# Kernel tuning notes

Measured on AMD Instinct MI355X. Metric: run time of the kernel, lower is better.

## Reference

```python
import jax, jax.numpy as jnp
import numpy as np

NUM_HEADS = 8
EPS = 1e-12  # torch F.normalize eps


def setup_inputs() -> dict:
    key = jax.random.key(0)
    k1, k2, k3 = jax.random.split(key, 3)
    B, N, C = 8, 4096, 768
    x = jax.random.normal(k1, (B, N, C), dtype=jnp.float32)
    Wqkv = jax.random.normal(k2, (C, 3 * C), dtype=jnp.float32) * 0.02
    temperature = jnp.ones((NUM_HEADS, 1, 1), dtype=jnp.float32)
    Wproj = jax.random.normal(k3, (C, C), dtype=jnp.float32) * 0.02
    bproj = jnp.zeros((C,), dtype=jnp.float32)
    return {"x": x, "Wqkv": Wqkv, "temperature": temperature,
            "Wproj": Wproj, "bproj": bproj}


def _l2norm(t):
    # torch F.normalize(dim=-1): x / max(||x||, eps)
    n = jnp.sqrt(jnp.sum(t * t, axis=-1, keepdims=True))
    return t / jnp.maximum(n, EPS)


def reference(x, Wqkv, temperature, Wproj, bproj):
    B, N, C = x.shape
    H = NUM_HEADS
    Ch = C // H
    qkv = (x @ Wqkv).reshape(B, N, 3, H, Ch)
    qkv = qkv.transpose(2, 0, 3, 1, 4)           # (3, B, H, N, Ch)
    q, k, v = qkv[0], qkv[1], qkv[2]
    # transpose(-2,-1): attend over channels -> (B, H, Ch, N)
    q = jnp.swapaxes(q, -2, -1)
    k = jnp.swapaxes(k, -2, -1)
    v = jnp.swapaxes(v, -2, -1)
    q = _l2norm(q)
    k = _l2norm(k)
    # (B, H, Ch, Ch) channel-attention scores, scaled by learned temperature
    attn = jnp.einsum('bhcn,bhdn->bhcd', q, k) * temperature
    attn = jax.nn.softmax(attn, axis=-1)
    out = jnp.einsum('bhcd,bhdn->bhcn', attn, v)  # (B, H, Ch, N)
    out = out.transpose(0, 3, 1, 2).reshape(B, N, C)
    return out @ Wproj + bproj
```

## Files before the change

### kernel.cpp

```cpp
#include <hip/hip_runtime.h>
#include <cstdint>
#include <cstddef>

typedef unsigned short u16;
typedef short bf16x8 __attribute__((ext_vector_type(8)));
typedef unsigned short u16x4 __attribute__((ext_vector_type(4)));
typedef unsigned short u16x8 __attribute__((ext_vector_type(8)));
typedef float f32x4 __attribute__((ext_vector_type(4)));

#define EPSN 1e-12f

__device__ __forceinline__ u16 f2bf(float f) {
  uint32_t u = __builtin_bit_cast(uint32_t, f);
  u += 0x7FFFu + ((u >> 16) & 1u);
  return (u16)(u >> 16);
}
__device__ __forceinline__ float bf2f(u16 h) {
  uint32_t u = ((uint32_t)h) << 16;
  return __builtin_bit_cast(float, u);
}

__device__ __forceinline__ void gll16(const u16* g, u16* l) {
  __builtin_amdgcn_global_load_lds(
      (const __attribute__((address_space(1))) void*)g,
      (__attribute__((address_space(3))) void*)l, 16, 0, 0);
}

__global__ __launch_bounds__(256)
void k_cvtT(const float* __restrict__ x, u16* __restrict__ Xh,
            u16* __restrict__ XhT) {
  __shared__ u16 tr[64][68];
  const int tid = threadIdx.x;
  const int t0 = blockIdx.x * 64, k0 = blockIdx.y * 64, b = blockIdx.z;
  const size_t base = ((size_t)b * 4096 + t0) * 768 + k0;
#pragma unroll
  for (int p = 0; p < 4; p++) {
    const int r = (tid >> 4) + p * 16;
    const int c = (tid & 15) * 4;
    f32x4 v = *(const f32x4*)(x + base + (size_t)r * 768 + c);
    u16x4 o;
#pragma unroll
    for (int e = 0; e < 4; e++) o[e] = f2bf(v[e]);
    *(u16x4*)(Xh + base + (size_t)r * 768 + c) = o;
    tr[c + 0][r] = o[0];
    tr[c + 1][r] = o[1];
    tr[c + 2][r] = o[2];
    tr[c + 3][r] = o[3];
  }
  __syncthreads();
  const size_t tbase = ((size_t)b * 768 + k0) * 4096 + t0;
#pragma unroll
  for (int p = 0; p < 4; p++) {
    const int kk = (tid >> 4) + p * 16;
    const int ts = (tid & 15) * 4;
    u16x4 o;
#pragma unroll
    for (int e = 0; e < 4; e++) o[e] = tr[kk][ts + e];
    *(u16x4*)(XhT + tbase + (size_t)kk * 4096 + ts) = o;
  }
}

__global__ __launch_bounds__(256)
void k_wt(const float* __restrict__ W, u16* __restrict__ Wt, u16* __restrict__ Wvh) {
  __shared__ float tile[32][33];
  const int j0 = blockIdx.x * 32;
  const int k0 = blockIdx.y * 32;
  const int tx = threadIdx.x & 31;
  const int ty = threadIdx.x >> 5;
#pragma unroll
  for (int r = 0; r < 4; r++) {
    float v = W[(size_t)(k0 + ty + r * 8) * 2304 + j0 + tx];
    tile[ty + r * 8][tx] = v;
    if (j0 >= 1536)
      Wvh[(size_t)(k0 + ty + r * 8) * 768 + (j0 - 1536) + tx] = f2bf(v);
  }
  __syncthreads();
  if (j0 < 1536) {
#pragma unroll
    for (int r = 0; r < 4; r++)
      Wt[(size_t)(j0 + ty + r * 8) * 768 + k0 + tx] = f2bf(tile[tx][ty + r * 8]);
  }
}

template <int OUTF32B, int TRI>
__global__ __launch_bounds__(256, 3)
void k_gemm(const u16* __restrict__ A, const u16* __restrict__ Btp,
            void* __restrict__ Cp, const float* __restrict__ bias,
            int K, int lda, int ldb, int ldc,
            long aZ, long bZ, long cZ, int zK, long kss) {
  const int gx = gridDim.x, gy = gridDim.y;
  int f = blockIdx.x + gx * (blockIdx.y + gy * blockIdx.z);
  const int total = gx * gy * gridDim.z;
  const int q = total >> 3, rr = total & 7;
  const int xcd = f & 7, kk0 = f >> 3;
  f = (xcd < rr ? xcd * (q + 1) : rr * (q + 1) + (xcd - rr) * q) + kk0;
  const int bx = f % gx;
  const int tmp = f / gx;
  const int by = tmp % gy;
  const int bz = tmp / gy;

  int m0, n0;
  if constexpr (TRI) {
    const int ty = (bx >= 20) ? 5 : (bx >= 18) ? 4 : (bx >= 15) ? 3
                 : (bx >= 11) ? 2 : (bx >= 6) ? 1 : 0;
    const int txi = ty + (bx - (ty * 6 - (ty * (ty - 1)) / 2));
    m0 = ty * 128;
    n0 = txi * 128;
  } else {
    m0 = by * 128;
    n0 = bx * 128;
  }
  const int z = bz;
  const int bb = z / zK, ss = z % zK;
  const u16* Az = A + (long)bb * aZ + (long)ss * kss;
  const u16* Btz = Btp + (long)bb * bZ + (long)ss * kss;

  __shared__ u16 As[128 * 32];
  __shared__ u16 Bs[128 * 32];
  const int tid = threadIdx.x;
  const int lane = tid & 63;
  const int wid = tid >> 6;
  const int wr = wid >> 1, wc = wid & 1;
  const int fm = lane & 15, kg = lane >> 4;

  const int lr = lane >> 2;
  const int gk = (lane & 3) ^ ((lane >> 3) & 3);
  const u16* gA0 = Az + (size_t)(m0 + wid * 32 + lr) * lda + gk * 8;
  const u16* gA1 = gA0 + (size_t)16 * lda;
  const u16* gB0 = Btz + (size_t)(n0 + wid * 32 + lr) * ldb + gk * 8;
  const u16* gB1 = gB0 + (size_t)16 * ldb;
  u16* lA0 = As + wid * 1024;
  u16* lA1 = lA0 + 512;
  u16* lB0 = Bs + wid * 1024;
  u16* lB1 = lB0 + 512;
  const int kq = (kg ^ ((fm >> 1) & 3)) * 8;

  f32x4 acc[4][4] = {};
  for (int k0 = 0; k0 < K; k0 += 32) {
    __syncthreads();
    gll16(gA0, lA0);
    gll16(gA1, lA1);
    gll16(gB0, lB0);
    gll16(gB1, lB1);
    gA0 += 32; gA1 += 32; gB0 += 32; gB1 += 32;
    __syncthreads();
    bf16x8 af[4], bfr[4];
#pragma unroll
    for (int i = 0; i < 4; i++)
      af[i] = *(const bf16x8*)&As[(wr * 64 + i * 16 + fm) * 32 + kq];
#pragma unroll
    for (int j = 0; j < 4; j++)
      bfr[j] = *(const bf16x8*)&Bs[(wc * 64 + j * 16 + fm) * 32 + kq];
#pragma unroll
    for (int i = 0; i < 4; i++)
#pragma unroll
      for (int j = 0; j < 4; j++)
        acc[i][j] = __builtin_amdgcn_mfma_f32_16x16x32_bf16(af[i], bfr[j], acc[i][j], 0, 0, 0);
  }

  if constexpr (OUTF32B) {
    float* C = (float*)Cp + (long)z * cZ;
#pragma unroll
    for (int j = 0; j < 4; j++) {
      const int col = n0 + wc * 64 + j * 16 + fm;
      const float bj = bias[col];
#pragma unroll
      for (int i = 0; i < 4; i++) {
        const int r0 = m0 + wr * 64 + i * 16 + kg * 4;
#pragma unroll
        for (int r = 0; r < 4; r++)
          C[(size_t)(r0 + r) * ldc + col] = acc[i][j][r] + bj;
      }
    }
  } else {
    const int rb = TRI ? 0 : m0;
    const int cb = TRI ? 0 : n0;
    const int ld = TRI ? 128 : ldc;
    u16* C = (u16*)Cp + (long)z * cZ + (TRI ? (long)bx * 16384 : 0L);
#pragma unroll
    for (int j = 0; j < 4; j++) {
      const int col = cb + wc * 64 + j * 16 + fm;
#pragma unroll
      for (int i = 0; i < 4; i++) {
        const int r0 = rb + wr * 64 + i * 16 + kg * 4;
#pragma unroll
        for (int r = 0; r < 4; r++)
          C[(size_t)(r0 + r) * ld + col] = f2bf(acc[i][j][r]);
      }
    }
  }
}

__global__ __launch_bounds__(256)
void k_red(const u16* __restrict__ P, u16* __restrict__ O) {
  const int b = blockIdx.y;
  const int ti = blockIdx.x / 6, tj = blockIdx.x % 6;
  const bool mirror = ti > tj;
  const int a = mirror ? tj : ti;
  const int c2 = mirror ? ti : tj;
  const int src = a * 6 - (a * (a - 1)) / 2 + (c2 - a);
  __shared__ u16 lt[128 * 128];
  const int tid = threadIdx.x;
  const int r = tid >> 1;
  const int ch = (tid & 1) * 64;
  float acc[64] = {};
  for (int s = 0; s < 4; s++) {
    const u16* p = P + ((size_t)(b * 4 + s) * 344064 + (size_t)src * 16384);
    __syncthreads();
#pragma unroll
    for (int it = 0; it < 8; it++) {
      const int idx = (tid + it * 256) * 8;
      *(u16x8*)&lt[idx] = *(const u16x8*)(p + idx);
    }
    __syncthreads();
    if (!mirror) {
#pragma unroll
      for (int e = 0; e < 64; e++) acc[e] += bf2f(lt[r * 128 + ch + e]);
    } else {
#pragma unroll
      for (int e = 0; e < 64; e++) acc[e] += bf2f(lt[(ch + e) * 128 + r]);
    }
  }
  u16* o = O + (size_t)b * 589824 + (size_t)(ti * 128 + r) * 768 + tj * 128 + ch;
#pragma unroll
  for (int v8 = 0; v8 < 8; v8++) {
    u16x8 w;
#pragma unroll
    for (int e = 0; e < 8; e++) w[e] = f2bf(acc[v8 * 8 + e]);
    *(u16x8*)(o + v8 * 8) = w;
  }
}

__global__ __launch_bounds__(256)
void k_score(const u16* __restrict__ Tm, const u16* __restrict__ Wt,
             const float* __restrict__ temperature, float* __restrict__ Aattn) {
  const int h = blockIdx.x, b = blockIdx.y;
  const int bh = b * 8 + h;
  __shared__ u16 As[96 * 32];
  __shared__ u16 Bs[96 * 32];
  __shared__ u16 Dt2[96 * 32];
  __shared__ u16 Dwq[96 * 32];
  __shared__ float Gs[96 * 96];
  __shared__ float nqs[96], nks[96], invk[96];

  const int tid = threadIdx.x;
  const int lane = tid & 63;
  const int wid = tid >> 6;
  const int wr = wid >> 1, wc = wid & 1;
  const int fm = lane & 15, kg = lane >> 4;
  const int lr = lane >> 2;
  const int gkS = (lane & 3) ^ ((lane >> 3) & 3);
  const int gkL = (lane & 3);
  const int kq = (kg ^ ((fm >> 1) & 3)) * 8;

  const u16* baseT1 = Tm + (size_t)b * 1179648 + (size_t)(h * 96) * 768;
  const u16* baseT2 = baseT1 + (size_t)768 * 768;
  const u16* baseWq = Wt + (size_t)(h * 96) * 768;
  const u16* baseWk = baseWq + (size_t)768 * 768;

  const u16* gsrc;
  u16* ldst;
  int gblk = gkS;
  if (wid == 0) { gsrc = baseT1; ldst = As; }
  else if (wid == 1) { gsrc = baseWk; ldst = Bs; }
  else if (wid == 2) { gsrc = baseT2; ldst = Dt2; gblk = gkL; }
  else { gsrc = baseWq; ldst = Dwq; gblk = gkL; }

  f32x4 acc[3][3] = {};
  float nqa = 0.f, nka = 0.f;
  const int sw1 = (tid < 96) ? ((tid >> 1) & 3) : 0;
  const int sw2 = (tid >= 128 && tid < 224) ? (((tid - 128) >> 1) & 3) : 0;

  for (int k0 = 0; k0 < 768; k0 += 32) {
    __syncthreads();
#pragma unroll
    for (int c = 0; c < 6; c++) {
      gll16(gsrc + (size_t)(c * 16 + lr) * 768 + k0 + gblk * 8,
            ldst + c * 512);
    }
    __syncthreads();
    bf16x8 af[3], bfr[3];
#pragma unroll
    for (int i = 0; i < 3; i++)
      af[i] = *(const bf16x8*)&As[(wr * 48 + i * 16 + fm) * 32 + kq];
#pragma unroll
    for (int j = 0; j < 3; j++)
      bfr[j] = *(const bf16x8*)&Bs[(wc * 48 + j * 16 + fm) * 32 + kq];
#pragma unroll
    for (int i = 0; i < 3; i++)
#pragma unroll
      for (int j = 0; j < 3; j++)
        acc[i][j] = __builtin_amdgcn_mfma_f32_16x16x32_bf16(af[i], bfr[j], acc[i][j], 0, 0, 0);
    if (tid < 96) {
#pragma unroll
      for (int g = 0; g < 4; g++) {
        u16x8 av = *(const u16x8*)&As[tid * 32 + (g ^ sw1) * 8];
        u16x8 w = *(const u16x8*)&Dwq[tid * 32 + g * 8];
#pragma unroll
        for (int e = 0; e < 8; e++) nqa += bf2f(av[e]) * bf2f(w[e]);
      }
    } else if (tid >= 128 && tid < 224) {
      const int d = tid - 128;
#pragma unroll
      for (int g = 0; g < 4; g++) {
        u16x8 av = *(const u16x8*)&Bs[d * 32 + (g ^ sw2) * 8];
        u16x8 w = *(const u16x8*)&Dt2[d * 32 + g * 8];
#pragma unroll
        for (int e = 0; e < 8; e++) nka += bf2f(av[e]) * bf2f(w[e]);
      }
    }
  }

  if (tid < 96) nqs[tid] = nqa;
  if (tid >= 128 && tid < 224) nks[tid - 128] = nka;
#pragma unroll
  for (int i = 0; i < 3; i++)
#pragma unroll
    for (int j = 0; j < 3; j++)
#pragma unroll
      for (int r = 0; r < 4; r++)
        Gs[(wr * 48 + i * 16 + kg * 4 + r) * 96 + wc * 48 + j * 16 + fm] = acc[i][j][r];
  __syncthreads();
  if (tid < 96) invk[tid] = 1.0f / fmaxf(sqrtf(nks[tid]), EPSN);
  __syncthreads();
  if (tid < 96) {
    const int c = tid;
    const float iq = temperature[h] / fmaxf(sqrtf(nqs[c]), EPSN);
    float sv[96];
    float m = -1e30f;
#pragma unroll
    for (int d = 0; d < 96; d++) {
      float s = Gs[c * 96 + d] * iq * invk[d];
      sv[d] = s;
      m = fmaxf(m, s);
    }
    float sum = 0.f;
#pragma unroll
    for (int d = 0; d < 96; d++) {
      float e = __expf(sv[d] - m);
      sv[d] = e;
      sum += e;
    }
    const float inv = 1.0f / sum;
    float* dst = Aattn + (size_t)bh * 9216 + (size_t)c * 96;
#pragma unroll
    for (int d = 0; d < 96; d++) dst[d] = sv[d] * inv;
  }
}

__global__ __launch_bounds__(256)
void k_weff(const float* __restrict__ Aattn, const float* __restrict__ Wproj,
            u16* __restrict__ Weff) {
  const int jt = blockIdx.x, h = blockIdx.y, b = blockIdx.z;
  const int bh = b * 8 + h;
  __shared__ float As2[9216];
  const int tid = threadIdx.x;
  for (int idx = tid; idx < 9216; idx += 256)
    As2[idx] = Aattn[(size_t)bh * 9216 + idx];
  __syncthreads();
  const int jloc = tid & 127;
  const int half = tid >> 7;
  const int j = jt * 128 + jloc;
  float acc[48] = {};
  for (int c = 0; c < 96; c++) {
    const float w = Wproj[(size_t)(h * 96 + c) * 768 + j];
    const f32x4* ar = (const f32x4*)&As2[c * 96 + half * 48];
#pragma unroll
    for (int v4 = 0; v4 < 12; v4++) {
      f32x4 av = ar[v4];
      acc[v4 * 4 + 0] += w * av[0];
      acc[v4 * 4 + 1] += w * av[1];
      acc[v4 * 4 + 2] += w * av[2];
      acc[v4 * 4 + 3] += w * av[3];
    }
  }
  u16* dst = Weff + ((size_t)b * 768 + j) * 768 + h * 96 + half * 48;
#pragma unroll
  for (int v4 = 0; v4 < 12; v4++) {
    u16x4 o;
    o[0] = f2bf(acc[v4 * 4 + 0]);
    o[1] = f2bf(acc[v4 * 4 + 1]);
    o[2] = f2bf(acc[v4 * 4 + 2]);
    o[3] = f2bf(acc[v4 * 4 + 3]);
    *(u16x4*)(dst + v4 * 4) = o;
  }
}

extern "C" void kernel_launch(void* const* d_in, const int* in_sizes, int n_in,
                              void* d_out, int out_size, void* d_ws, size_t ws_size,
                              hipStream_t stream) {
  const float* x = (const float*)d_in[0];
  const float* Wqkv = (const float*)d_in[1];
  const float* temp = (const float*)d_in[2];
  const float* Wproj = (const float*)d_in[3];
  const float* bproj = (const float*)d_in[4];
  float* out = (float*)d_out;

  char* ws = (char*)d_ws;
  u16* Xh = (u16*)ws;
  u16* XhT = (u16*)(ws + 50331648);
  u16* Wt = (u16*)(ws + 100663296);
  u16* Wvh = (u16*)(ws + 103022592);
  u16* XtXp = (u16*)(ws + 104202240);
  u16* XtXbf = (u16*)(ws + 141950976);
  u16* T = (u16*)(ws + 151388160);
  u16* WeffT = (u16*)(ws + 151388160);
  u16* WcompT = (u16*)(ws + 160825344);
  float* Aattn = (float*)(ws + 170262528);

  k_cvtT<<<dim3(64, 12, 8), 256, 0, stream>>>(x, Xh, XhT);
  k_wt<<<dim3(72, 24), 256, 0, stream>>>(Wqkv, Wt, Wvh);
  k_gemm<0, 1><<<dim3(21, 1, 32), 256, 0, stream>>>(
      XhT, XhT, (void*)XtXp, nullptr, 1024, 4096, 4096, 0,
      3145728L, 3145728L, 344064L, 4, 1024L);
  k_red<<<dim3(36, 8), 256, 0, stream>>>(XtXp, XtXbf);
  k_gemm<0, 0><<<dim3(6, 12, 8), 256, 0, stream>>>(
      Wt, XtXbf, (void*)T, nullptr, 768, 768, 768, 768,
      0L, 589824L, 1179648L, 1, 0L);
  k_score<<<dim3(8, 8), 256, 0, stream>>>(T, Wt, temp, Aattn);
  k_weff<<<dim3(6, 8, 8), 256, 0, stream>>>(Aattn, Wproj, WeffT);
  k_gemm<0, 0><<<dim3(6, 6, 8), 256, 0, stream>>>(
      WeffT, Wvh, (void*)WcompT, nullptr, 768, 768, 768, 768,
      589824L, 0L, 589824L, 1, 0L);
  k_gemm<1, 0><<<dim3(6, 32, 8), 256, 0, stream>>>(
      Xh, WcompT, out, bproj, 768, 768, 768, 768,
      3145728L, 589824L, 3145728L, 1, 0L);
}
```

Baseline: 304.5 us.

## Triple-buffer LDS tiles in bf16 GEMM to overlap global loads with MFMA

Replaces the single-buffered LDS staging in the GEMM kernel with a three-slot ring buffer. Tiles for k-step t+2 are prefetched with global_load_lds while step t is computed, and explicit vmcnt waits plus barriers replace the old pair of syncthreads. The aim is to hide global memory latency behind the matrix instructions, at the cost of three times the shared memory per block, which can lower occupancy.

```diff
diff --git a/kernel.cpp b/kernel.cpp
--- a/kernel.cpp
+++ b/kernel.cpp
@@ -115,8 +115,8 @@
   const u16* Az = A + (long)bb * aZ + (long)ss * kss;
   const u16* Btz = Btp + (long)bb * bZ + (long)ss * kss;
 
-  __shared__ u16 As[128 * 32];
-  __shared__ u16 Bs[128 * 32];
+  __shared__ u16 As[3 * 128 * 32];
+  __shared__ u16 Bs[3 * 128 * 32];
   const int tid = threadIdx.x;
   const int lane = tid & 63;
   const int wid = tid >> 6;
@@ -125,37 +125,63 @@
 
   const int lr = lane >> 2;
   const int gk = (lane & 3) ^ ((lane >> 3) & 3);
-  const u16* gA0 = Az + (size_t)(m0 + wid * 32 + lr) * lda + gk * 8;
-  const u16* gA1 = gA0 + (size_t)16 * lda;
-  const u16* gB0 = Btz + (size_t)(n0 + wid * 32 + lr) * ldb + gk * 8;
-  const u16* gB1 = gB0 + (size_t)16 * ldb;
-  u16* lA0 = As + wid * 1024;
-  u16* lA1 = lA0 + 512;
-  u16* lB0 = Bs + wid * 1024;
-  u16* lB1 = lB0 + 512;
+  const u16* gA = Az + (size_t)(m0 + wid * 32 + lr) * lda + gk * 8;
+  const u16* gB = Btz + (size_t)(n0 + wid * 32 + lr) * ldb + gk * 8;
+  const size_t a16 = (size_t)16 * lda, b16 = (size_t)16 * ldb;
+  u16* lA = As + wid * 1024;
+  u16* lB = Bs + wid * 1024;
   const int kq = (kg ^ ((fm >> 1) & 3)) * 8;
 
+  auto STAGE = [&](int slot, int ko) {
+    u16* la = lA + slot * 4096;
+    u16* lb = lB + slot * 4096;
+    gll16(gA + ko, la);
+    gll16(gA + ko + a16, la + 512);
+    gll16(gB + ko, lb);
+    gll16(gB + ko + b16, lb + 512);
+  };
+
+  const int nt = K >> 5;
+  STAGE(0, 0);
+  STAGE(1, 32);
+  int sC = 0, sN = 1, sS = 2;
+
   f32x4 acc[4][4] = {};
-  for (int k0 = 0; k0 < K; k0 += 32) {
-    __syncthreads();
-    gll16(gA0, lA0);
-    gll16(gA1, lA1);
-    gll16(gB0, lB0);
-    gll16(gB1, lB1);
-    gA0 += 32; gA1 += 32; gB0 += 32; gB1 += 32;
-    __syncthreads();
+  for (int t = 0; t < nt; ++t) {
+    if (t + 2 < nt) {
+      STAGE(sS, (t + 2) * 32);
+      __builtin_amdgcn_sched_barrier(0);
+      asm volatile("s_waitcnt vmcnt(8)" ::: "memory");
+    } else if (t + 2 == nt) {
+      asm volatile("s_waitcnt vmcnt(4)" ::: "memory");
+    } else {
+      asm volatile("s_waitcnt vmcnt(0)" ::: "memory");
+    }
+    __builtin_amdgcn_sched_barrier(0);
+    __builtin_amdgcn_s_barrier();
+    __builtin_amdgcn_sched_barrier(0);
+
+    const u16* as_ = As + sC * 4096;
+    const u16* bs_ = Bs + sC * 4096;
     bf16x8 af[4], bfr[4];
 #pragma unroll
     for (int i = 0; i < 4; i++)
-      af[i] = *(const bf16x8*)&As[(wr * 64 + i * 16 + fm) * 32 + kq];
+      af[i] = *(const bf16x8*)&as_[(wr * 64 + i * 16 + fm) * 32 + kq];
 #pragma unroll
     for (int j = 0; j < 4; j++)
-      bfr[j] = *(const bf16x8*)&Bs[(wc * 64 + j * 16 + fm) * 32 + kq];
+      bfr[j] = *(const bf16x8*)&bs_[(wc * 64 + j * 16 + fm) * 32 + kq];
+    asm volatile("s_waitcnt lgkmcnt(0)" ::: "memory");
+    __builtin_amdgcn_sched_barrier(0);
+    __builtin_amdgcn_s_barrier();
+    __builtin_amdgcn_sched_barrier(0);
+
 #pragma unroll
     for (int i = 0; i < 4; i++)
 #pragma unroll
       for (int j = 0; j < 4; j++)
         acc[i][j] = __builtin_amdgcn_mfma_f32_16x16x32_bf16(af[i], bfr[j], acc[i][j], 0, 0, 0);
+
+    const int t2 = sC; sC = sN; sN = sS; sS = t2;
   }
 
   if constexpr (OUTF32B) {
```

Result: faster. 297.2 us (-2.4%).
